# Optimization experiments

Hardware: AMD Instinct MI355X
Metric: run time of the kernel (lower is better)

Reference implementation:

```python
import jax, jax.numpy as jnp
import numpy as np

# 3x3 laplacian stencil, OIHW
LAP = jnp.array([-1, -1, -1, -1, 8, -1, -1, -1, -1], dtype=jnp.float32).reshape(1, 1, 3, 3)
THR = 0.1
SMOOTH = 1.0


def _lap_conv(x, stride):
    # x: [B,1,H,W]
    return jax.lax.conv_general_dilated(
        x, LAP, window_strides=(stride, stride), padding=((1, 1), (1, 1)),
        dimension_numbers=('NCHW', 'OIHW', 'NCHW'))


def _nearest_up(x, H, W):
    # PyTorch 'nearest': src_idx = floor(dst_idx * in/out)
    h, w = x.shape[2], x.shape[3]
    ri = (jnp.arange(H) * h) // H
    ci = (jnp.arange(W) * w) // W
    return x[:, :, ri][:, :, :, ci]


def _thresh(x):
    return jnp.where(x > THR, 1.0, 0.0).astype(x.dtype)


def setup_inputs() -> dict:
    key = jax.random.key(0)
    k1, k2 = jax.random.split(key)
    B, H, W = 16, 1024, 1024
    boundary_logits = jax.random.normal(k1, (B, 1, H, W), dtype=jnp.float32)
    gtmasks = (jax.random.uniform(k2, (B, H, W)) > 0.5).astype(jnp.float32)
    fuse_kernel = jnp.array([0.6, 0.3, 0.1], dtype=jnp.float32).reshape(1, 3, 1, 1)
    return {"boundary_logits": boundary_logits, "gtmasks": gtmasks, "fuse_kernel": fuse_kernel}


def reference(boundary_logits, gtmasks, fuse_kernel):
    g = gtmasks[:, None, :, :].astype(jnp.float32)  # [B,1,H,W]
    bt = _thresh(jnp.maximum(_lap_conv(g, 1), 0.0))  # full res
    H, W = bt.shape[2], bt.shape[3]
    bt2 = _thresh(_nearest_up(jnp.maximum(_lap_conv(g, 2), 0.0), H, W))
    bt4 = _thresh(_nearest_up(jnp.maximum(_lap_conv(g, 4), 0.0), H, W))
    # (x8 branch in original is computed but unused in the output)
    pyr = jnp.concatenate([bt, bt2, bt4], axis=1)  # [B,3,H,W]
    fused = jnp.einsum('bchw,c->bhw', pyr, fuse_kernel.reshape(3))[:, None]  # 1x1 fuse conv
    target = _thresh(fused)  # [B,1,H,W]

    x = boundary_logits
    # stable BCE with logits, mean reduction
    bce_loss = jnp.mean(jnp.maximum(x, 0.0) - x * target + jnp.log1p(jnp.exp(-jnp.abs(x))))

    p = jax.nn.sigmoid(x)
    n = p.shape[0]
    pf = p.reshape(n, -1)
    tf = target.reshape(n, -1)
    inter = jnp.sum(pf * tf, axis=1)
    dice_loss = jnp.mean(1.0 - (2.0 * inter + SMOOTH) / (jnp.sum(pf, 1) + jnp.sum(tf, 1) + SMOOTH))
    return bce_loss, dice_loss
```

## Files before the change

### kernel.cpp

```cpp
#include <hip/hip_runtime.h>

#define IMG_H 1024
#define IMG_W 1024
#define NIMG  16
#define NPIX  16777216.0f
#define SPI   128
#define NBLK  2048
#define LOG2E 1.44269504088896340736f
#define LN2   0.69314718055994530942f


__global__ __launch_bounds__(256, 3) void dal_main(
    const float* __restrict__ xlogits,
    const float* __restrict__ gmask,
    const float* __restrict__ fuse,
    float4* __restrict__ ws4)
{
    const int bid  = blockIdx.x;
    const int img  = bid >> 7;
    const int q    = bid & 127;
    const int r0   = q << 3;
    const int tid  = (int)threadIdx.x;
    const int lane = tid & 63;
    const int j0   = tid * 4;

    const float w0 = fuse[0], w1 = fuse[1], w2 = fuse[2];

    const size_t ibase = (size_t)img * (IMG_H * IMG_W);
    const float* gi = gmask + ibase;
    const float* xi = xlogits + ibase;

    const int  jl   = (j0 > 0) ? (j0 - 1) : 0;
    const int  jr1  = (j0 + 4 < IMG_W) ? (j0 + 1) : (IMG_W - 4);
    const bool hasL = (j0 > 0);
    const bool hasR = (j0 + 4 < IMG_W);

    float4 ga[10], gb[10];
    #pragma unroll
    for (int t = 0; t < 10; ++t) {
        int r  = r0 - 1 + t;
        int rc = r < 0 ? 0 : (r > IMG_H - 1 ? IMG_H - 1 : r);
        const float* row = gi + (size_t)rc * IMG_W;
        ga[t] = *reinterpret_cast<const float4*>(row + jl);
        gb[t] = *reinterpret_cast<const float4*>(row + jr1);
    }
    const float* xrow = xi + (size_t)r0 * IMG_W + j0;
    float4 xv[8];
    #pragma unroll
    for (int r = 0; r < 8; ++r)
        xv[r] = *reinterpret_cast<const float4*>(xrow + (size_t)r * IMG_W);

    float rm[10][4];
    float cv[8][4];
    #pragma unroll
    for (int t = 0; t < 10; ++t) {
        float c0 = hasL ? ga[t].x : 0.f;
        float c1 = hasL ? ga[t].y : ga[t].x;
        float c2 = hasL ? ga[t].z : ga[t].y;
        float c3 = hasL ? ga[t].w : ga[t].z;
        float c4 = hasR ? gb[t].z : gb[t].w;
        float c5 = hasR ? gb[t].w : 0.f;
        rm[t][0] = fminf(c0, fminf(c1, c2));
        rm[t][1] = fminf(c1, fminf(c2, c3));
        rm[t][2] = fminf(c2, fminf(c3, c4));
        rm[t][3] = fminf(c3, fminf(c4, c5));
        if (t >= 1 && t <= 8) {
            cv[t - 1][0] = c1; cv[t - 1][1] = c2;
            cv[t - 1][2] = c3; cv[t - 1][3] = c4;
        }
    }
    if (r0 == 0)          { rm[0][0] = rm[0][1] = rm[0][2] = rm[0][3] = 0.f; }
    if (r0 == IMG_H - 8)  { rm[9][0] = rm[9][1] = rm[9][2] = rm[9][3] = 0.f; }

    float bt[8][4];
    #pragma unroll
    for (int r = 0; r < 8; ++r)
        #pragma unroll
        for (int k = 0; k < 4; ++k) {
            float cm = fminf(rm[r][k], fminf(rm[r + 1][k], rm[r + 2][k]));
            bt[r][k] = (cv[r][k] > 0.5f && cm < 0.5f) ? 1.f : 0.f;
        }

    const float wb4A = w2 * bt[0][0];
    const float wb4B = w2 * bt[4][0];
    float base2[4][2];
    #pragma unroll
    for (int rp = 0; rp < 4; ++rp) {
        const float wb = (rp < 2) ? wb4A : wb4B;
        base2[rp][0] = fmaf(w1, bt[2 * rp][0], wb);
        base2[rp][1] = fmaf(w1, bt[2 * rp][2], wb);
    }

    float l2[2]  = {0.f, 0.f}, xt[2] = {0.f, 0.f};
    float itr[2] = {0.f, 0.f}, sp[2] = {0.f, 0.f};
    int st = 0;

    auto px = [&](float x, float btv, float b2v, int a) {
        float f = fmaf(w0, btv, b2v);
        bool  c = f > 0.1f;
        st += (int)__popcll(__ballot(c));
        float u   = __builtin_amdgcn_exp2f(x * LOG2E);
        float opu = 1.f + u;
        float p   = u * __builtin_amdgcn_rcpf(opu);
        l2[a]  += __builtin_amdgcn_logf(opu);
        sp[a]  += p;
        xt[a]  += c ? x : 0.f;
        itr[a] += c ? p : 0.f;
    };

    #pragma unroll
    for (int r = 0; r < 8; ++r) {
        const int   rp = r >> 1;
        const int   a  = r & 1;
        const float bA = base2[rp][0];
        const float bB = base2[rp][1];
        px(xv[r].x, bt[r][0], bA, a);
        px(xv[r].y, bt[r][1], bA, a);
        px(xv[r].z, bt[r][2], bB, a);
        px(xv[r].w, bt[r][3], bB, a);
    }

    float bce   = fmaf(LN2, l2[0] + l2[1], -(xt[0] + xt[1]));
    float inter = itr[0] + itr[1];
    float sump  = sp[0] + sp[1];

    #pragma unroll
    for (int off = 32; off > 0; off >>= 1) {
        bce   += __shfl_down(bce, off);
        inter += __shfl_down(inter, off);
        sump  += __shfl_down(sump, off);
    }
    __shared__ float red[4][4];
    const int wid = tid >> 6;
    if (lane == 0) {
        red[0][wid] = bce; red[1][wid] = inter;
        red[2][wid] = sump; red[3][wid] = (float)st;
    }
    __syncthreads();
    if (tid == 0) {
        float4 o;
        o.x = red[0][0] + red[0][1] + red[0][2] + red[0][3];
        o.y = red[1][0] + red[1][1] + red[1][2] + red[1][3];
        o.z = red[2][0] + red[2][1] + red[2][2] + red[2][3];
        o.w = red[3][0] + red[3][1] + red[3][2] + red[3][3];
        ws4[bid] = o;
    }
}

__global__ __launch_bounds__(1024) void dal_finalize(
    const float4* __restrict__ ws4, float* __restrict__ out)
{
    const int t    = (int)threadIdx.x;
    const int wv   = t >> 6;
    const int lane = t & 63;

    float4 a = ws4[2 * t];
    float4 b = ws4[2 * t + 1];
    float bce   = a.x + b.x;
    float inter = a.y + b.y;
    float sump  = a.z + b.z;
    float sumt  = a.w + b.w;

    #pragma unroll
    for (int off = 32; off > 0; off >>= 1) {
        bce   += __shfl_down(bce, off);
        inter += __shfl_down(inter, off);
        sump  += __shfl_down(sump, off);
        sumt  += __shfl_down(sumt, off);
    }

    __shared__ float sb[16], sd[16];
    if (lane == 0) {
        sb[wv] = bce;
        sd[wv] = 1.f - (2.f * inter + 1.f) / (sump + sumt + 1.f);
    }
    __syncthreads();
    if (t == 0) {
        float tb = 0.f, td = 0.f;
        #pragma unroll
        for (int i = 0; i < NIMG; ++i) { tb += sb[i]; td += sd[i]; }
        out[0] = tb / NPIX;
        out[1] = td / (float)NIMG;
    }
}

extern "C" void kernel_launch(void* const* d_in, const int* in_sizes, int n_in,
                              void* d_out, int out_size, void* d_ws, size_t ws_size,
                              hipStream_t stream)
{
    const float* x    = (const float*)d_in[0];
    const float* g    = (const float*)d_in[1];
    const float* fuse = (const float*)d_in[2];
    float* out = (float*)d_out;
    float4* ws4 = (float4*)d_ws;

    dal_main<<<NBLK, 256, 0, stream>>>(x, g, fuse, ws4);
    dal_finalize<<<1, 1024, 0, stream>>>(ws4, out);
}
```

Before: 31.55 us.

## Software-pipeline row strips with double-buffered register loads per block

Each block now processes four 4-row strips of one image, spaced 64 strips apart, instead of a single 8-row strip. The loads for the next strip are issued into a second register buffer before the current strip is computed, so memory latency overlaps with compute. The grid is halved and the finalize kernel reads one partial per thread. In exchange, each 4-row strip needs 6 mask rows, so more halo rows are re-read, register pressure rises, and the occupancy hint drops from 3 to 2.

```diff
diff --git a/kernel.cpp b/kernel.cpp
--- a/kernel.cpp
+++ b/kernel.cpp
@@ -4,22 +4,21 @@
 #define IMG_W 1024
 #define NIMG  16
 #define NPIX  16777216.0f
-#define SPI   128
-#define NBLK  2048
+#define NBLK  1024
+#define KSTR  4
 #define LOG2E 1.44269504088896340736f
 #define LN2   0.69314718055994530942f
 
 
-__global__ __launch_bounds__(256, 3) void dal_main(
+__global__ __launch_bounds__(256, 2) void dal_main(
     const float* __restrict__ xlogits,
     const float* __restrict__ gmask,
     const float* __restrict__ fuse,
     float4* __restrict__ ws4)
 {
-    const int bid  = blockIdx.x;
-    const int img  = bid >> 7;
-    const int q    = bid & 127;
-    const int r0   = q << 3;
+    const int b    = blockIdx.x;
+    const int img  = b >> 6;
+    const int qb   = b & 63;
     const int tid  = (int)threadIdx.x;
     const int lane = tid & 63;
     const int j0   = tid * 4;
@@ -35,65 +34,28 @@
     const bool hasL = (j0 > 0);
     const bool hasR = (j0 + 4 < IMG_W);
 
-    float4 ga[10], gb[10];
-    #pragma unroll
-    for (int t = 0; t < 10; ++t) {
-        int r  = r0 - 1 + t;
-        int rc = r < 0 ? 0 : (r > IMG_H - 1 ? IMG_H - 1 : r);
-        const float* row = gi + (size_t)rc * IMG_W;
-        ga[t] = *reinterpret_cast<const float4*>(row + jl);
-        gb[t] = *reinterpret_cast<const float4*>(row + jr1);
-    }
-    const float* xrow = xi + (size_t)r0 * IMG_W + j0;
-    float4 xv[8];
-    #pragma unroll
-    for (int r = 0; r < 8; ++r)
-        xv[r] = *reinterpret_cast<const float4*>(xrow + (size_t)r * IMG_W);
-
-    float rm[10][4];
-    float cv[8][4];
-    #pragma unroll
-    for (int t = 0; t < 10; ++t) {
-        float c0 = hasL ? ga[t].x : 0.f;
-        float c1 = hasL ? ga[t].y : ga[t].x;
-        float c2 = hasL ? ga[t].z : ga[t].y;
-        float c3 = hasL ? ga[t].w : ga[t].z;
-        float c4 = hasR ? gb[t].z : gb[t].w;
-        float c5 = hasR ? gb[t].w : 0.f;
-        rm[t][0] = fminf(c0, fminf(c1, c2));
-        rm[t][1] = fminf(c1, fminf(c2, c3));
-        rm[t][2] = fminf(c2, fminf(c3, c4));
-        rm[t][3] = fminf(c3, fminf(c4, c5));
-        if (t >= 1 && t <= 8) {
-            cv[t - 1][0] = c1; cv[t - 1][1] = c2;
-            cv[t - 1][2] = c3; cv[t - 1][3] = c4;
-        }
-    }
-    if (r0 == 0)          { rm[0][0] = rm[0][1] = rm[0][2] = rm[0][3] = 0.f; }
-    if (r0 == IMG_H - 8)  { rm[9][0] = rm[9][1] = rm[9][2] = rm[9][3] = 0.f; }
-
-    float bt[8][4];
-    #pragma unroll
-    for (int r = 0; r < 8; ++r)
-        #pragma unroll
-        for (int k = 0; k < 4; ++k) {
-            float cm = fminf(rm[r][k], fminf(rm[r + 1][k], rm[r + 2][k]));
-            bt[r][k] = (cv[r][k] > 0.5f && cm < 0.5f) ? 1.f : 0.f;
-        }
-
-    const float wb4A = w2 * bt[0][0];
-    const float wb4B = w2 * bt[4][0];
-    float base2[4][2];
-    #pragma unroll
-    for (int rp = 0; rp < 4; ++rp) {
-        const float wb = (rp < 2) ? wb4A : wb4B;
-        base2[rp][0] = fmaf(w1, bt[2 * rp][0], wb);
-        base2[rp][1] = fmaf(w1, bt[2 * rp][2], wb);
-    }
+    float4 gaA[6], gbA[6], xvA[4];
+    float4 gaB[6], gbB[6], xvB[4];
 
     float l2[2]  = {0.f, 0.f}, xt[2] = {0.f, 0.f};
     float itr[2] = {0.f, 0.f}, sp[2] = {0.f, 0.f};
     int st = 0;
+
+    auto issue = [&](int q, float4 (&ga)[6], float4 (&gb)[6], float4 (&xv)[4]) {
+        const int r0 = q << 2;
+        #pragma unroll
+        for (int t = 0; t < 6; ++t) {
+            int r  = r0 - 1 + t;
+            int rc = r < 0 ? 0 : (r > IMG_H - 1 ? IMG_H - 1 : r);
+            const float* row = gi + (size_t)rc * IMG_W;
+            ga[t] = *reinterpret_cast<const float4*>(row + jl);
+            gb[t] = *reinterpret_cast<const float4*>(row + jr1);
+        }
+        const float* xr = xi + (size_t)r0 * IMG_W + j0;
+        #pragma unroll
+        for (int r = 0; r < 4; ++r)
+            xv[r] = *reinterpret_cast<const float4*>(xr + (size_t)r * IMG_W);
+    };
 
     auto px = [&](float x, float btv, float b2v, int a) {
         float f = fmaf(w0, btv, b2v);
@@ -108,16 +70,66 @@
         itr[a] += c ? p : 0.f;
     };
 
+    auto compute = [&](int q, float4 (&ga)[6], float4 (&gb)[6], float4 (&xv)[4]) {
+        const int r0 = q << 2;
+        float rm[6][4], cv[4][4];
+        #pragma unroll
+        for (int t = 0; t < 6; ++t) {
+            float c0 = hasL ? ga[t].x : 0.f;
+            float c1 = hasL ? ga[t].y : ga[t].x;
+            float c2 = hasL ? ga[t].z : ga[t].y;
+            float c3 = hasL ? ga[t].w : ga[t].z;
+            float c4 = hasR ? gb[t].z : gb[t].w;
+            float c5 = hasR ? gb[t].w : 0.f;
+            rm[t][0] = fminf(c0, fminf(c1, c2));
+            rm[t][1] = fminf(c1, fminf(c2, c3));
+            rm[t][2] = fminf(c2, fminf(c3, c4));
+            rm[t][3] = fminf(c3, fminf(c4, c5));
+            if (t >= 1 && t <= 4) {
+                cv[t - 1][0] = c1; cv[t - 1][1] = c2;
+                cv[t - 1][2] = c3; cv[t - 1][3] = c4;
+            }
+        }
+        if (r0 == 0)         { rm[0][0] = rm[0][1] = rm[0][2] = rm[0][3] = 0.f; }
+        if (r0 == IMG_H - 4) { rm[5][0] = rm[5][1] = rm[5][2] = rm[5][3] = 0.f; }
+
+        float bt[4][4];
+        #pragma unroll
+        for (int r = 0; r < 4; ++r)
+            #pragma unroll
+            for (int k = 0; k < 4; ++k) {
+                float cm = fminf(rm[r][k], fminf(rm[r + 1][k], rm[r + 2][k]));
+                bt[r][k] = (cv[r][k] > 0.5f && cm < 0.5f) ? 1.f : 0.f;
+            }
+
+        const float wb4 = w2 * bt[0][0];
+        float base2[2][2];
+        base2[0][0] = fmaf(w1, bt[0][0], wb4);
+        base2[0][1] = fmaf(w1, bt[0][2], wb4);
+        base2[1][0] = fmaf(w1, bt[2][0], wb4);
+        base2[1][1] = fmaf(w1, bt[2][2], wb4);
+
+        #pragma unroll
+        for (int r = 0; r < 4; ++r) {
+            const float bA = base2[r >> 1][0];
+            const float bB = base2[r >> 1][1];
+            px(xv[r].x, bt[r][0], bA, r & 1);
+            px(xv[r].y, bt[r][1], bA, r & 1);
+            px(xv[r].z, bt[r][2], bB, r & 1);
+            px(xv[r].w, bt[r][3], bB, r & 1);
+        }
+    };
+
+    issue(qb, gaA, gbA, xvA);
     #pragma unroll
-    for (int r = 0; r < 8; ++r) {
-        const int   rp = r >> 1;
-        const int   a  = r & 1;
-        const float bA = base2[rp][0];
-        const float bB = base2[rp][1];
-        px(xv[r].x, bt[r][0], bA, a);
-        px(xv[r].y, bt[r][1], bA, a);
-        px(xv[r].z, bt[r][2], bB, a);
-        px(xv[r].w, bt[r][3], bB, a);
+    for (int k = 0; k < KSTR; ++k) {
+        if ((k & 1) == 0) {
+            if (k < KSTR - 1) issue(qb + 64 * (k + 1), gaB, gbB, xvB);
+            compute(qb + 64 * k, gaA, gbA, xvA);
+        } else {
+            if (k < KSTR - 1) issue(qb + 64 * (k + 1), gaA, gbA, xvA);
+            compute(qb + 64 * k, gaB, gbB, xvB);
+        }
     }
 
     float bce   = fmaf(LN2, l2[0] + l2[1], -(xt[0] + xt[1]));
@@ -143,7 +155,7 @@
         o.y = red[1][0] + red[1][1] + red[1][2] + red[1][3];
         o.z = red[2][0] + red[2][1] + red[2][2] + red[2][3];
         o.w = red[3][0] + red[3][1] + red[3][2] + red[3][3];
-        ws4[bid] = o;
+        ws4[b] = o;
     }
 }
 
@@ -154,12 +166,11 @@
     const int wv   = t >> 6;
     const int lane = t & 63;
 
-    float4 a = ws4[2 * t];
-    float4 b = ws4[2 * t + 1];
-    float bce   = a.x + b.x;
-    float inter = a.y + b.y;
-    float sump  = a.z + b.z;
-    float sumt  = a.w + b.w;
+    float4 a = ws4[t];
+    float bce   = a.x;
+    float inter = a.y;
+    float sump  = a.z;
+    float sumt  = a.w;
 
     #pragma unroll
     for (int off = 32; off > 0; off >>= 1) {
```

New measurement: 37.50 us. 18.8% more time.
